# Kernel optimization log

Hardware: AMD Instinct MI355X
Metric: run time of the kernel (lower is better)

Reference implementation:

```python
import jax, jax.numpy as jnp
import numpy as np

N_NODES = 50000
N_EDGES = 800000
N_GRAPHS = 2500
IN_DIM = 128
HID = 64
HEADS = 2
NEG_SLOPE = 0.2


def _gat_layer(x, W, att_src, att_dst, bias, src, dst, n):
    # W: [F_in, H*C], att_*: [H, C], bias: [C]
    h = (x @ W).reshape(n, HEADS, HID)            # [N,H,C]
    a_src = jnp.sum(h * att_src[None], axis=-1)   # [N,H]
    a_dst = jnp.sum(h * att_dst[None], axis=-1)   # [N,H]
    e = jax.nn.leaky_relu(a_src[src] + a_dst[dst], NEG_SLOPE)  # [E,H]
    # segment softmax over destination neighborhoods
    m = jax.ops.segment_max(e, dst, num_segments=n)            # [N,H]
    m = jnp.where(jnp.isfinite(m), m, 0.0)
    ex = jnp.exp(e - m[dst])
    s = jax.ops.segment_sum(ex, dst, num_segments=n)           # [N,H]
    alpha = ex / jnp.maximum(s[dst], 1e-16)                    # [E,H]
    msg = h[src] * alpha[:, :, None]                           # [E,H,C]
    out = jax.ops.segment_sum(msg, dst, num_segments=n)        # [N,H,C]
    return out.mean(axis=1) + bias                             # concat=False -> head mean


def _with_self_loops(edge_index, n):
    loop = jnp.arange(n, dtype=edge_index.dtype)
    src = jnp.concatenate([edge_index[0], loop])
    dst = jnp.concatenate([edge_index[1], loop])
    return src, dst


def setup_inputs() -> dict:
    key = jax.random.key(0)
    ks = jax.random.split(key, 16)
    x = jax.random.normal(ks[0], (N_NODES, IN_DIM), dtype=jnp.float32)
    edge_index = jax.random.randint(ks[1], (2, N_EDGES), 0, N_NODES, dtype=jnp.int32)
    batch = jnp.sort(jax.random.randint(ks[2], (N_NODES,), 0, N_GRAPHS, dtype=jnp.int32))

    def glorot(k, shape):
        fan = shape[0] + shape[-1]
        return jax.random.normal(k, shape, dtype=jnp.float32) * np.sqrt(2.0 / fan)

    inp = {"x": x, "edge_index": edge_index, "batch": batch}
    dims = [IN_DIM, HID, HID]
    for i in range(3):
        inp[f"W{i+1}"] = glorot(ks[3 + 4 * i], (dims[i], HEADS * HID))
        inp[f"att_src{i+1}"] = glorot(ks[4 + 4 * i], (HEADS, HID))
        inp[f"att_dst{i+1}"] = glorot(ks[5 + 4 * i], (HEADS, HID))
        inp[f"b{i+1}"] = jnp.zeros((HID,), dtype=jnp.float32)
    inp["lin_w"] = glorot(ks[15], (HID, 1))
    inp["lin_b"] = jnp.zeros((1,), dtype=jnp.float32)
    return inp


def reference(x, W1, att_src1, att_dst1, b1, W2, att_src2, att_dst2, b2,
              W3, att_src3, att_dst3, b3, lin_w, lin_b, edge_index, batch):
    n = x.shape[0]
    src, dst = _with_self_loops(edge_index, n)
    h = jax.nn.relu(_gat_layer(x, W1, att_src1, att_dst1, b1, src, dst, n))
    h = jax.nn.relu(_gat_layer(h, W2, att_src2, att_dst2, b2, src, dst, n))
    h = jax.nn.relu(_gat_layer(h, W3, att_src3, att_dst3, b3, src, dst, n))
    # global mean pool over graphs
    sums = jax.ops.segment_sum(h, batch, num_segments=N_GRAPHS)          # [G,C]
    cnt = jax.ops.segment_sum(jnp.ones((n,), h.dtype), batch, num_segments=N_GRAPHS)
    pooled = sums / jnp.maximum(cnt, 1.0)[:, None]
    return pooled @ lin_w + lin_b                                        # [G,1]
```

## Files before the change

### kernel.cpp

```cpp
#include <hip/hip_runtime.h>
#include <hip/hip_fp16.h>
#include <math.h>


__device__ __forceinline__ float lrelu(float v) { return v > 0.f ? v : 0.2f * v; }

__device__ __forceinline__ float wave_max(float v) {
  for (int off = 32; off; off >>= 1) v = fmaxf(v, __shfl_xor(v, off, 64));
  return v;
}
__device__ __forceinline__ float half_sum(float v) {
  for (int off = 16; off; off >>= 1) v += __shfl_xor(v, off, 64);
  return v;
}
__device__ __forceinline__ float half_max(float v) {
  for (int off = 16; off; off >>= 1) v = fmaxf(v, __shfl_xor(v, off, 64));
  return v;
}

typedef _Float16 f16x8 __attribute__((ext_vector_type(8)));
typedef float f32x4 __attribute__((ext_vector_type(4)));

__device__ __forceinline__ int colperm(int l, int ks) {
  return l == 0 ? ks : (((ks & 3) << 4) | ((ks >> 3) << 1) | ((ks >> 2) & 1));
}

__global__ void count_rank_prep(const int* __restrict__ ei, int* __restrict__ deg,
                                int* __restrict__ rank, int e, int eb,
                                const float* __restrict__ W1, const float* __restrict__ as1,
                                const float* __restrict__ ad1,
                                const float* __restrict__ W2, const float* __restrict__ as2,
                                const float* __restrict__ ad2,
                                const float* __restrict__ W3, const float* __restrict__ as3,
                                const float* __restrict__ ad3,
                                __half* __restrict__ WT1, __half* __restrict__ WT2,
                                __half* __restrict__ WT3,
                                const int* __restrict__ batch, const float* __restrict__ lb,
                                float* __restrict__ gcnt, float* __restrict__ gout,
                                int nn, int G) {
  int bx = blockIdx.x;
  int tid = threadIdx.x;
  if (bx < eb) {
    int j0 = bx * 1024 + tid;
#pragma unroll
    for (int k = 0; k < 4; ++k) {
      int j = j0 + k * 256;
      if (j < e) rank[j] = atomicAdd(&deg[ei[e + j]], 1);
    }
    return;
  }
  int pb = bx - eb;
  if (pb >= 24) {
    int pc = pb - 24;
    if (pc == 0) {
      float lb0 = lb[0];
      for (int g = tid; g < G; g += 256) gout[g] = lb0;
    }
    int j0 = pc * 1024 + tid;
#pragma unroll
    for (int k = 0; k < 4; ++k) {
      int i = j0 + k * 256;
      if (i < nn) atomicAdd(&gcnt[batch[i]], 1.0f);
    }
    return;
  }
  int l = pb >> 3, part = pb & 7;
  const float* W = l == 0 ? W1 : (l == 1 ? W2 : W3);
  const float* as = l == 0 ? as1 : (l == 1 ? as2 : as3);
  const float* ad = l == 0 ? ad1 : (l == 1 ? ad2 : ad3);
  __half* WT = l == 0 ? WT1 : (l == 1 ? WT2 : WT3);
  const int shk = l == 0 ? 7 : 6;
  const int K = 1 << shk;
  for (int idx = part * 256 + tid; idx < 144 * K; idx += 2048) {
    int row = idx >> shk;
    int ks = idx & (K - 1);
    int kt = colperm(l, ks);
    float val;
    if (row < 128) {
      val = W[kt * 128 + row];
    } else if (row < 132) {
      int j = row - 128;
      const float* att = (j < 2 ? as : ad) + (j & 1) * 64;
      const float* wr = W + kt * 128 + (j & 1) * 64;
      float acc = 0.f;
#pragma unroll
      for (int c = 0; c < 64; ++c) acc = fmaf(wr[c], att[c], acc);
      val = acc;
    } else {
      val = 0.f;
    }
    WT[idx] = __float2half(val);
  }
}

__global__ void scan_blocks(const int* __restrict__ deg, int* __restrict__ row_ptr,
                            int* __restrict__ btot, int n) {
  __shared__ int sm[256];
  int i = blockIdx.x * 256 + threadIdx.x;
  int v = (i < n) ? deg[i] : 0;
  sm[threadIdx.x] = v;
  __syncthreads();
  for (int off = 1; off < 256; off <<= 1) {
    int t = (threadIdx.x >= off) ? sm[threadIdx.x - off] : 0;
    __syncthreads();
    sm[threadIdx.x] += t;
    __syncthreads();
  }
  if (i < n) row_ptr[i] = sm[threadIdx.x] - v;
  if (threadIdx.x == 255) btot[blockIdx.x] = sm[255];
}

__global__ void scan_add2(int* __restrict__ row_ptr, int* __restrict__ csr,
                          const int* __restrict__ btot, int n, int total, int nb) {
  __shared__ int sm[256];
  int v = (threadIdx.x < nb) ? btot[threadIdx.x] : 0;
  sm[threadIdx.x] = v;
  __syncthreads();
  for (int off = 1; off < 256; off <<= 1) {
    int t = (threadIdx.x >= off) ? sm[threadIdx.x - off] : 0;
    __syncthreads();
    sm[threadIdx.x] += t;
    __syncthreads();
  }
  int base = sm[blockIdx.x] - btot[blockIdx.x];
  int i = blockIdx.x * 256 + threadIdx.x;
  if (i < n) {
    int v2 = row_ptr[i] + base + i;
    row_ptr[i] = v2;
    csr[v2] = i;
  }
  if (i == 0) row_ptr[n] = total;
}

__global__ void place_kernel(const int* __restrict__ ei, const int* __restrict__ rank,
                             const int* __restrict__ row_ptr, int* __restrict__ csr,
                             int e) {
  int j0 = blockIdx.x * 1024 + threadIdx.x;
#pragma unroll
  for (int k = 0; k < 4; ++k) {
    int j = j0 + k * 256;
    if (j < e) {
      int d = ei[e + j];
      csr[row_ptr[d] + 1 + rank[j]] = ei[j];
    }
  }
}

template <int K, bool F16IN>
__global__ __launch_bounds__(256) void gemm_mfma(const void* __restrict__ Xv,
                                                 const __half* __restrict__ WT,
                                                 __half* __restrict__ H16,
                                                 float* __restrict__ a_src,
                                                 float* __restrict__ a_dst, int N) {
  constexpr int KP = K + 8;
  extern __shared__ __half smem[];
  __half* Al = smem;
  __half* Wl = smem + 64 * KP;
  int tid = threadIdx.x;
  int row0 = blockIdx.x * 64;

  if constexpr (F16IN) {
    const __half* X = (const __half*)Xv;
    constexpr int CH = K / 8;
    for (int idx = tid; idx < 64 * CH; idx += 256) {
      int r = idx / CH, ch = idx % CH;
      int gr = row0 + r; if (gr >= N) gr = N - 1;
      *(uint4*)&Al[r * KP + ch * 8] = *(const uint4*)(X + (size_t)gr * K + ch * 8);
    }
  } else {
    const float* X = (const float*)Xv;
    constexpr int CH4 = K / 4;
    for (int idx = tid; idx < 64 * CH4; idx += 256) {
      int r = idx / CH4, ch = idx % CH4;
      int gr = row0 + r; if (gr >= N) gr = N - 1;
      float4 v = *(const float4*)(X + (size_t)gr * K + ch * 4);
      union { __half2 h2[2]; uint2 u; } t;
      t.h2[0] = __floats2half2_rn(v.x, v.y);
      t.h2[1] = __floats2half2_rn(v.z, v.w);
      *(uint2*)&Al[r * KP + ch * 4] = t.u;
    }
  }
  constexpr int CHW = K / 8;
  for (int idx = tid; idx < 144 * CHW; idx += 256) {
    int r = idx / CHW, ch = idx % CHW;
    *(uint4*)&Wl[r * KP + ch * 8] = *(const uint4*)(WT + r * K + ch * 8);
  }
  __syncthreads();

  int lane = tid & 63;
  int wv = tid >> 6;
  int q = lane & 15;
  int kg = lane >> 4;

  f32x4 acc[9] = {};
  const __half* ap = &Al[(wv * 16 + q) * KP + kg * 8];
  const __half* wp = &Wl[q * KP + kg * 8];
#pragma unroll
  for (int ks = 0; ks < K / 32; ++ks) {
    f16x8 a = *(const f16x8*)(ap + ks * 32);
#pragma unroll
    for (int n = 0; n < 9; ++n) {
      f16x8 b = *(const f16x8*)(wp + n * 16 * KP + ks * 32);
      acc[n] = __builtin_amdgcn_mfma_f32_16x16x32_f16(a, b, acc[n], 0, 0, 0);
    }
  }

#pragma unroll
  for (int reg = 0; reg < 4; ++reg) {
    int r = row0 + wv * 16 + kg * 4 + reg;
    if (r < N) {
      union { __half2 h2[2]; uint2 u; } s0, s1;
      s0.h2[0] = __floats2half2_rn(acc[0][reg], acc[1][reg]);
      s0.h2[1] = __floats2half2_rn(acc[2][reg], acc[3][reg]);
      s1.h2[0] = __floats2half2_rn(acc[4][reg], acc[5][reg]);
      s1.h2[1] = __floats2half2_rn(acc[6][reg], acc[7][reg]);
      *(uint2*)(H16 + (size_t)r * 128 + q * 4) = s0.u;
      *(uint2*)(H16 + (size_t)r * 128 + 64 + q * 4) = s1.u;
      float av = acc[8][reg];
      if (q < 2) a_src[r * 2 + q] = av;
      else if (q < 4) a_dst[r * 2 + q - 2] = av;
    }
  }
}

__device__ __forceinline__ void ld_grp8(const __half* __restrict__ H16, int half_,
                                        int c8, int headsel, int sub, int s,
                                        float p0, float p1, int g,
                                        uint4* h, float* q) {
#pragma unroll
  for (int k = 0; k < 4; ++k) {
    int idx = half_ + g * 8 + k * 2 + sub;
    int st = __shfl(s, idx, 64);
    float q0 = __shfl(p0, idx, 64);
    float q1 = __shfl(p1, idx, 64);
    q[k] = headsel ? q1 : q0;
    h[k] = *(const uint4*)(H16 + (size_t)st * 128 + c8);
  }
}
__device__ __forceinline__ void fma_grp8(const uint4* h, const float* q,
                                         float* acc) {
#pragma unroll
  for (int k = 0; k < 4; ++k) {
    union { uint u; __half2 h2; } a, b, c, d;
    a.u = h[k].x; b.u = h[k].y; c.u = h[k].z; d.u = h[k].w;
    float2 f0 = __half22float2(a.h2);
    float2 f1 = __half22float2(b.h2);
    float2 f2 = __half22float2(c.h2);
    float2 f3 = __half22float2(d.h2);
    acc[0] = fmaf(f0.x, q[k], acc[0]);
    acc[1] = fmaf(f0.y, q[k], acc[1]);
    acc[2] = fmaf(f1.x, q[k], acc[2]);
    acc[3] = fmaf(f1.y, q[k], acc[3]);
    acc[4] = fmaf(f2.x, q[k], acc[4]);
    acc[5] = fmaf(f2.y, q[k], acc[5]);
    acc[6] = fmaf(f3.x, q[k], acc[6]);
    acc[7] = fmaf(f3.y, q[k], acc[7]);
  }
}
__device__ __forceinline__ void gather_pipe8(const __half* __restrict__ H16, int half_,
                                             int c8, int headsel, int sub, int s,
                                             float p0, float p1, int maxcnt,
                                             float* acc) {
  int groups = (maxcnt + 7) >> 3;
  uint4 ha[4], hb[4];
  float qa[4], qb[4];
  ld_grp8(H16, half_, c8, headsel, sub, s, p0, p1, 0, ha, qa);
  int g = 1;
  for (; g + 1 < groups; g += 2) {
    ld_grp8(H16, half_, c8, headsel, sub, s, p0, p1, g, hb, qb);
    fma_grp8(ha, qa, acc);
    ld_grp8(H16, half_, c8, headsel, sub, s, p0, p1, g + 1, ha, qa);
    fma_grp8(hb, qb, acc);
  }
  if (g < groups) {
    ld_grp8(H16, half_, c8, headsel, sub, s, p0, p1, g, hb, qb);
    fma_grp8(ha, qa, acc);
    fma_grp8(hb, qb, acc);
  } else {
    fma_grp8(ha, qa, acc);
  }
}

template <int POOL>
__global__ __launch_bounds__(256) void aggregate_fused(
    const __half* __restrict__ H16, const float* __restrict__ a_src,
    const float* __restrict__ a_dst, const float* __restrict__ bias,
    const int* __restrict__ row_ptr, const int* __restrict__ csr,
    __half* __restrict__ out, const float* __restrict__ lw,
    const int* __restrict__ batch, const float* __restrict__ gcnt,
    float* __restrict__ gout, int N) {
  int lane = threadIdx.x & 63;
  int half_ = lane & 32;
  int l32 = lane & 31;
  int dst = blockIdx.x * 8 + ((threadIdx.x >> 6) << 1) + (half_ >> 5);
  bool live = dst < N;
  int beg = live ? row_ptr[dst] : 0;
  int end = live ? row_ptr[dst + 1] : 0;
  int cnt = end - beg;
  float2 ad = live ? ((const float2*)a_dst)[dst] : make_float2(0.f, 0.f);
  int sub = l32 >> 4;
  int m = l32 & 15;
  int c8 = m * 8;
  int headsel = m >> 3;
  float acc[8] = {};
  float inv0, inv1;

  int maxcnt = (int)wave_max((float)cnt);
  if (maxcnt < 1) maxcnt = 1;

  if (maxcnt <= 32) {
    int j = beg + l32;
    bool valid = l32 < cnt;
    int s = valid ? csr[j] : 0;
    float2 as = ((const float2*)a_src)[s];
    float e0 = valid ? lrelu(as.x + ad.x) : -1e30f;
    float e1 = valid ? lrelu(as.y + ad.y) : -1e30f;
    float m0 = half_max(e0);
    float m1 = half_max(e1);
    float p0 = __expf(e0 - m0);
    float p1 = __expf(e1 - m1);
    inv0 = 1.f / fmaxf(half_sum(valid ? p0 : 0.f), 1e-16f);
    inv1 = 1.f / fmaxf(half_sum(valid ? p1 : 0.f), 1e-16f);
    gather_pipe8(H16, half_, c8, headsel, sub, s, p0, p1, maxcnt, acc);
  } else {
    float m0 = -1e30f, m1 = -1e30f, s0 = 0.f, s1 = 0.f;
    for (int base = 0; base < maxcnt; base += 32) {
      int j = beg + base + l32;
      bool valid = (base + l32) < cnt;
      int s = valid ? csr[j] : 0;
      float2 as = ((const float2*)a_src)[s];
      float e0 = valid ? lrelu(as.x + ad.x) : -1e30f;
      float e1 = valid ? lrelu(as.y + ad.y) : -1e30f;
      float nm0 = fmaxf(m0, half_max(e0));
      float nm1 = fmaxf(m1, half_max(e1));
      s0 = s0 * __expf(m0 - nm0) + half_sum(valid ? __expf(e0 - nm0) : 0.f);
      s1 = s1 * __expf(m1 - nm1) + half_sum(valid ? __expf(e1 - nm1) : 0.f);
      m0 = nm0; m1 = nm1;
    }
    inv0 = 1.f / fmaxf(s0, 1e-16f);
    inv1 = 1.f / fmaxf(s1, 1e-16f);
    for (int base = 0; base < maxcnt; base += 32) {
      int j = beg + base + l32;
      bool valid = (base + l32) < cnt;
      int s = valid ? csr[j] : 0;
      float2 as = ((const float2*)a_src)[s];
      float e0 = valid ? lrelu(as.x + ad.x) : -1e30f;
      float e1 = valid ? lrelu(as.y + ad.y) : -1e30f;
      float p0 = __expf(e0 - m0);
      float p1 = __expf(e1 - m1);
      int rem = maxcnt - base;
      if (rem > 32) rem = 32;
      gather_pipe8(H16, half_, c8, headsel, sub, s, p0, p1, rem, acc);
    }
  }

#pragma unroll
  for (int j = 0; j < 8; ++j) acc[j] += __shfl_xor(acc[j], 16, 64);

  float il = headsel ? inv1 : inv0;
  float v[8], w[8];
#pragma unroll
  for (int j = 0; j < 8; ++j) v[j] = acc[j] * il;
#pragma unroll
  for (int j = 0; j < 8; ++j) w[j] = __shfl_xor(v[j], 8, 64);

  if (m < 8 && sub == 0 && live) {
    int cb = m << 1;
    float r[8];
#pragma unroll
    for (int j = 0; j < 8; ++j) {
      int c = ((j & 3) << 4) + cb + (j >> 2);
      r[j] = fmaxf(0.5f * (v[j] + w[j]) + bias[c], 0.f);
    }
    if (POOL) {
      float pv = 0.f;
#pragma unroll
      for (int j = 0; j < 8; ++j) {
        int c = ((j & 3) << 4) + cb + (j >> 2);
        pv = fmaf(r[j], lw[c], pv);
      }
      pv += __shfl_xor(pv, 1, 64);
      pv += __shfl_xor(pv, 2, 64);
      pv += __shfl_xor(pv, 4, 64);
      if (m == 0) {
        int bg = batch[dst];
        atomicAdd(&gout[bg], pv / fmaxf(gcnt[bg], 1.f));
      }
    } else {
      union { __half2 h2[4]; uint4 u; } pk;
      pk.h2[0] = __floats2half2_rn(r[0], r[1]);
      pk.h2[1] = __floats2half2_rn(r[2], r[3]);
      pk.h2[2] = __floats2half2_rn(r[4], r[5]);
      pk.h2[3] = __floats2half2_rn(r[6], r[7]);
      *(uint4*)(out + (size_t)dst * 64 + m * 8) = pk.u;
    }
  }
}

extern "C" void kernel_launch(void* const* d_in, const int* in_sizes, int n_in,
                              void* d_out, int out_size, void* d_ws, size_t ws_size,
                              hipStream_t stream) {
  const float* x   = (const float*)d_in[0];
  const int* ei    = (const int*)d_in[1];
  const int* batch = (const int*)d_in[2];
  const float* W1  = (const float*)d_in[3];
  const float* as1 = (const float*)d_in[4];
  const float* ad1 = (const float*)d_in[5];
  const float* b1  = (const float*)d_in[6];
  const float* W2  = (const float*)d_in[7];
  const float* as2 = (const float*)d_in[8];
  const float* ad2 = (const float*)d_in[9];
  const float* b2  = (const float*)d_in[10];
  const float* W3  = (const float*)d_in[11];
  const float* as3 = (const float*)d_in[12];
  const float* ad3 = (const float*)d_in[13];
  const float* b3  = (const float*)d_in[14];
  const float* lw  = (const float*)d_in[15];
  const float* lb  = (const float*)d_in[16];
  float* out = (float*)d_out;

  const int N = in_sizes[0] / 128;
  const int E = in_sizes[1] / 2;
  const int ET = N + E;
  const int G = out_size;
  const int NB = (N + 255) / 256;
  const int EB = (E + 1023) / 1024;
  const int CB = (N + 1023) / 1024;

  char* p = (char*)d_ws;
  auto take = [&](size_t bytes) {
    char* r = p;
    p += (bytes + 255) & ~(size_t)255;
    return r;
  };
  int* deg      = (int*)take((size_t)N * 4);
  float* gcnt   = (float*)take((size_t)G * 4);
  int* row_ptr  = (int*)take((size_t)(N + 1) * 4);
  int* rank     = (int*)take((size_t)E * 4);
  int* btot     = (int*)take((size_t)NB * 4);
  int* csr      = (int*)take((size_t)ET * 4);
  __half* H16   = (__half*)take((size_t)N * 128 * 2);
  float* a_src  = (float*)take((size_t)N * 2 * 4);
  float* a_dst  = (float*)take((size_t)N * 2 * 4);
  __half* bufA  = (__half*)take((size_t)N * 64 * 2);
  __half* bufB  = (__half*)take((size_t)N * 64 * 2);
  __half* WT1   = (__half*)take((size_t)144 * 128 * 2);
  __half* WT2   = (__half*)take((size_t)144 * 64 * 2);
  __half* WT3   = (__half*)take((size_t)144 * 64 * 2);
  (void)ws_size; (void)n_in;

  size_t zlen = (size_t)((char*)gcnt - (char*)deg) + (size_t)G * 4;
  hipMemsetAsync(deg, 0, zlen, stream);
  count_rank_prep<<<EB + 24 + CB, 256, 0, stream>>>(ei, deg, rank, E, EB,
                                                    W1, as1, ad1, W2, as2, ad2,
                                                    W3, as3, ad3, WT1, WT2, WT3,
                                                    batch, lb, gcnt, out, N, G);
  scan_blocks<<<NB, 256, 0, stream>>>(deg, row_ptr, btot, N);
  scan_add2<<<NB, 256, 0, stream>>>(row_ptr, csr, btot, N, ET, NB);
  place_kernel<<<EB, 256, 0, stream>>>(ei, rank, row_ptr, csr, E);

  const int gblk = (N + 63) / 64;
  const int ablk = (N + 7) / 8;
  constexpr int LDS1 = (64 + 144) * (128 + 8) * 2;
  constexpr int LDS2 = (64 + 144) * (64 + 8) * 2;

  gemm_mfma<128, false><<<gblk, 256, LDS1, stream>>>(x, WT1, H16, a_src, a_dst, N);
  aggregate_fused<0><<<ablk, 256, 0, stream>>>(H16, a_src, a_dst, b1, row_ptr, csr,
                                               bufA, lw, batch, gcnt, out, N);
  gemm_mfma<64, true><<<gblk, 256, LDS2, stream>>>(bufA, WT2, H16, a_src, a_dst, N);
  aggregate_fused<0><<<ablk, 256, 0, stream>>>(H16, a_src, a_dst, b2, row_ptr, csr,
                                               bufB, lw, batch, gcnt, out, N);
  gemm_mfma<64, true><<<gblk, 256, LDS2, stream>>>(bufB, WT3, H16, a_src, a_dst, N);
  aggregate_fused<1><<<ablk, 256, 0, stream>>>(H16, a_src, a_dst, b3, row_ptr, csr,
                                               bufA, lw, batch, gcnt, out, N);
}
```

Measured before the change: 317.3 us.

## Replace global atomic degree counting with partitioned LDS histograms per edge chunk

Measured after the change: 343.1 us. 8.1% more time.

```diff
diff --git a/kernel.cpp b/kernel.cpp
--- a/kernel.cpp
+++ b/kernel.cpp
@@ -21,35 +21,49 @@
 typedef _Float16 f16x8 __attribute__((ext_vector_type(8)));
 typedef float f32x4 __attribute__((ext_vector_type(4)));
 
+#define PARTSZ 6400
+#define NCHUNK 32
+
 __device__ __forceinline__ int colperm(int l, int ks) {
   return l == 0 ? ks : (((ks & 3) << 4) | ((ks >> 3) << 1) | ((ks >> 2) & 1));
 }
 
-__global__ void count_rank_prep(const int* __restrict__ ei, int* __restrict__ deg,
-                                int* __restrict__ rank, int e, int eb,
-                                const float* __restrict__ W1, const float* __restrict__ as1,
-                                const float* __restrict__ ad1,
-                                const float* __restrict__ W2, const float* __restrict__ as2,
-                                const float* __restrict__ ad2,
-                                const float* __restrict__ W3, const float* __restrict__ as3,
-                                const float* __restrict__ ad3,
-                                __half* __restrict__ WT1, __half* __restrict__ WT2,
-                                __half* __restrict__ WT3,
-                                const int* __restrict__ batch, const float* __restrict__ lb,
-                                float* __restrict__ gcnt, float* __restrict__ gout,
-                                int nn, int G) {
+__global__ void hist_rank_prep(const int* __restrict__ ei, int* __restrict__ rank,
+                               int* __restrict__ hist, int e, int cs, int P, int C,
+                               const float* __restrict__ W1, const float* __restrict__ as1,
+                               const float* __restrict__ ad1,
+                               const float* __restrict__ W2, const float* __restrict__ as2,
+                               const float* __restrict__ ad2,
+                               const float* __restrict__ W3, const float* __restrict__ as3,
+                               const float* __restrict__ ad3,
+                               __half* __restrict__ WT1, __half* __restrict__ WT2,
+                               __half* __restrict__ WT3,
+                               const int* __restrict__ batch, const float* __restrict__ lb,
+                               float* __restrict__ gcnt, float* __restrict__ gout,
+                               int nn, int G) {
+  __shared__ int h[PARTSZ];
   int bx = blockIdx.x;
   int tid = threadIdx.x;
-  if (bx < eb) {
-    int j0 = bx * 1024 + tid;
-#pragma unroll
-    for (int k = 0; k < 4; ++k) {
-      int j = j0 + k * 256;
-      if (j < e) rank[j] = atomicAdd(&deg[ei[e + j]], 1);
+  int PC = P * C;
+  if (bx < PC) {
+    int c = bx / P;
+    int part = bx - c * P;
+    int d0 = part * PARTSZ;
+    for (int i = tid; i < PARTSZ; i += 256) h[i] = 0;
+    __syncthreads();
+    int j1 = (c + 1) * cs; if (j1 > e) j1 = e;
+    for (int j = c * cs + tid; j < j1; j += 256) {
+      int d = ei[e + j] - d0;
+      if ((unsigned)d < (unsigned)PARTSZ) rank[j] = atomicAdd(&h[d], 1);
+    }
+    __syncthreads();
+    for (int i = tid; i < PARTSZ; i += 256) {
+      int d = d0 + i;
+      if (d < nn) hist[c * nn + d] = h[i];
     }
     return;
   }
-  int pb = bx - eb;
+  int pb = bx - PC;
   if (pb >= 24) {
     int pc = pb - 24;
     if (pc == 0) {
@@ -84,7 +98,7 @@
       const float* wr = W + kt * 128 + (j & 1) * 64;
       float acc = 0.f;
 #pragma unroll
-      for (int c = 0; c < 64; ++c) acc = fmaf(wr[c], att[c], acc);
+      for (int cc = 0; cc < 64; ++cc) acc = fmaf(wr[cc], att[cc], acc);
       val = acc;
     } else {
       val = 0.f;
@@ -93,12 +107,19 @@
   }
 }
 
-__global__ void scan_blocks(const int* __restrict__ deg, int* __restrict__ row_ptr,
-                            int* __restrict__ btot, int n) {
+__global__ void scan_blocks(int* __restrict__ hist, int* __restrict__ row_ptr,
+                            int* __restrict__ btot, int n, int C) {
   __shared__ int sm[256];
   int i = blockIdx.x * 256 + threadIdx.x;
-  int v = (i < n) ? deg[i] : 0;
-  sm[threadIdx.x] = v;
+  int deg = 0;
+  if (i < n) {
+    for (int c = 0; c < C; ++c) {
+      int hh = hist[c * n + i];
+      hist[c * n + i] = deg;
+      deg += hh;
+    }
+  }
+  sm[threadIdx.x] = deg;
   __syncthreads();
   for (int off = 1; off < 256; off <<= 1) {
     int t = (threadIdx.x >= off) ? sm[threadIdx.x - off] : 0;
@@ -106,7 +127,7 @@
     sm[threadIdx.x] += t;
     __syncthreads();
   }
-  if (i < n) row_ptr[i] = sm[threadIdx.x] - v;
+  if (i < n) row_ptr[i] = sm[threadIdx.x] - deg;
   if (threadIdx.x == 255) btot[blockIdx.x] = sm[255];
 }
 
@@ -133,15 +154,17 @@
 }
 
 __global__ void place_kernel(const int* __restrict__ ei, const int* __restrict__ rank,
-                             const int* __restrict__ row_ptr, int* __restrict__ csr,
-                             int e) {
+                             const int* __restrict__ row_ptr,
+                             const int* __restrict__ hist, int* __restrict__ csr,
+                             int e, int cs, int n) {
   int j0 = blockIdx.x * 1024 + threadIdx.x;
 #pragma unroll
   for (int k = 0; k < 4; ++k) {
     int j = j0 + k * 256;
     if (j < e) {
       int d = ei[e + j];
-      csr[row_ptr[d] + 1 + rank[j]] = ei[j];
+      int c = j / cs;
+      csr[row_ptr[d] + 1 + hist[c * n + d] + rank[j]] = ei[j];
     }
   }
 }
@@ -426,6 +449,8 @@
   const int NB = (N + 255) / 256;
   const int EB = (E + 1023) / 1024;
   const int CB = (N + 1023) / 1024;
+  const int P  = (N + PARTSZ - 1) / PARTSZ;
+  const int CS = (E + NCHUNK - 1) / NCHUNK;
 
   char* p = (char*)d_ws;
   auto take = [&](size_t bytes) {
@@ -433,12 +458,12 @@
     p += (bytes + 255) & ~(size_t)255;
     return r;
   };
-  int* deg      = (int*)take((size_t)N * 4);
   float* gcnt   = (float*)take((size_t)G * 4);
   int* row_ptr  = (int*)take((size_t)(N + 1) * 4);
   int* rank     = (int*)take((size_t)E * 4);
   int* btot     = (int*)take((size_t)NB * 4);
   int* csr      = (int*)take((size_t)ET * 4);
+  int* hist     = (int*)take((size_t)NCHUNK * N * 4);
   __half* H16   = (__half*)take((size_t)N * 128 * 2);
   float* a_src  = (float*)take((size_t)N * 2 * 4);
   float* a_dst  = (float*)take((size_t)N * 2 * 4);
@@ -449,15 +474,14 @@
   __half* WT3   = (__half*)take((size_t)144 * 64 * 2);
   (void)ws_size; (void)n_in;
 
-  size_t zlen = (size_t)((char*)gcnt - (char*)deg) + (size_t)G * 4;
-  hipMemsetAsync(deg, 0, zlen, stream);
-  count_rank_prep<<<EB + 24 + CB, 256, 0, stream>>>(ei, deg, rank, E, EB,
-                                                    W1, as1, ad1, W2, as2, ad2,
-                                                    W3, as3, ad3, WT1, WT2, WT3,
-                                                    batch, lb, gcnt, out, N, G);
-  scan_blocks<<<NB, 256, 0, stream>>>(deg, row_ptr, btot, N);
+  hipMemsetAsync(gcnt, 0, (size_t)G * 4, stream);
+  hist_rank_prep<<<P * NCHUNK + 24 + CB, 256, 0, stream>>>(
+      ei, rank, hist, E, CS, P, NCHUNK,
+      W1, as1, ad1, W2, as2, ad2, W3, as3, ad3, WT1, WT2, WT3,
+      batch, lb, gcnt, out, N, G);
+  scan_blocks<<<NB, 256, 0, stream>>>(hist, row_ptr, btot, N, NCHUNK);
   scan_add2<<<NB, 256, 0, stream>>>(row_ptr, csr, btot, N, ET, NB);
-  place_kernel<<<EB, 256, 0, stream>>>(ei, rank, row_ptr, csr, E);
+  place_kernel<<<EB, 256, 0, stream>>>(ei, rank, row_ptr, hist, csr, E, CS, N);
 
   const int gblk = (N + 63) / 64;
   const int ablk = (N + 7) / 8;
```
